# Kernel optimization log

Hardware: AMD Instinct MI355X
Metric: run time of the kernel (lower is better)

## Reference

```python
import jax, jax.numpy as jnp
import numpy as np

C = 256
R = 16  # reduction
CR = C // R
LN_EPS = 1e-5


def setup_inputs() -> dict:
    key = jax.random.key(0)
    ks = jax.random.split(key, 8)
    B, H, W = 16, 128, 128
    x = jax.random.normal(ks[0], (B, C, H, W), dtype=jnp.float32)
    # conv_mask: Conv2d(C, 1, 1x1)
    w_mask = jax.random.normal(ks[1], (C,), dtype=jnp.float32) * (1.0 / np.sqrt(C))
    b_mask = jnp.zeros((), dtype=jnp.float32)
    # channel_add[0]: Conv2d(C, C//R, 1x1)
    w1 = jax.random.normal(ks[2], (CR, C), dtype=jnp.float32) * (1.0 / np.sqrt(C))
    b1 = jnp.zeros((CR,), dtype=jnp.float32)
    # channel_add[1]: LayerNorm([C//R, 1, 1])
    ln_g = jnp.ones((CR,), dtype=jnp.float32)
    ln_b = jnp.zeros((CR,), dtype=jnp.float32)
    # channel_add[3]: Conv2d(C//R, C, 1x1)
    w2 = jax.random.normal(ks[3], (C, CR), dtype=jnp.float32) * (1.0 / np.sqrt(CR))
    b2 = jnp.zeros((C,), dtype=jnp.float32)
    return {"x": x, "w_mask": w_mask, "b_mask": b_mask,
            "w1": w1, "b1": b1, "ln_g": ln_g, "ln_b": ln_b,
            "w2": w2, "b2": b2}


def reference(x, w_mask, b_mask, w1, b1, ln_g, ln_b, w2, b2):
    B, Cc, H, W = x.shape
    # 1x1 conv to 1 channel -> attention logits over H*W
    logits = jnp.einsum('bchw,c->bhw', x, w_mask) + b_mask          # [B,H,W]
    attn = jax.nn.softmax(logits.reshape(B, H * W), axis=-1)        # [B,HW]
    # attention-pooled global context: [B,C]
    context = jnp.einsum('bchw,bs->bc', x, attn.reshape(B, H, W).reshape(B, H * W)[:, :].reshape(B, H * W)) if False else jnp.einsum('bcs,bs->bc', x.reshape(B, Cc, H * W), attn)
    # channel_add MLP: conv1x1 -> LayerNorm over [C//R] -> ReLU -> conv1x1
    t = jnp.einsum('oc,bc->bo', w1, context) + b1                   # [B,C//R]
    mu = jnp.mean(t, axis=-1, keepdims=True)
    var = jnp.mean((t - mu) ** 2, axis=-1, keepdims=True)
    t = (t - mu) / jnp.sqrt(var + LN_EPS) * ln_g + ln_b
    t = jax.nn.relu(t)
    add = jnp.einsum('oc,bc->bo', w2, t) + b2                       # [B,C]
    return x + add[:, :, None, None]
```

## Files before the change

kernel.cpp:

```cpp
#include <hip/hip_runtime.h>
#include <hip/hip_bf16.h>
#include <math.h>

#define CC   256
#define CR   16
#define SB   16384
#define NB   16
#define NCHUNK 64
#define CHSZ  256
#define ST   64
#define NT   (SB/ST)
#define LN_EPS 1e-5f

typedef float          vfloat4  __attribute__((ext_vector_type(4)));
typedef unsigned short vushort4 __attribute__((ext_vector_type(4)));

__device__ __forceinline__ unsigned short f2b(float f) {
    __hip_bfloat16 h = __float2bfloat16(f);
    unsigned short u;
    __builtin_memcpy(&u, &h, 2);
    return u;
}
__device__ __forceinline__ float b2f(unsigned short u) {
    unsigned int v = ((unsigned int)u) << 16;
    float f;
    __builtin_memcpy(&f, &v, 4);
    return f;
}

__global__ __launch_bounds__(256) void k1_shadow_part(const float* __restrict__ x,
                                                      const float* __restrict__ w_mask,
                                                      __hip_bfloat16* __restrict__ xb16,
                                                      float* __restrict__ part) {
    const int t   = threadIdx.x;
    const int bid = blockIdx.x;
    const int sq  = bid & 15;
    const int cg  = (bid >> 4) & 15;
    const int b   = bid >> 8;

    __shared__ float wm[16];
    if (t < 16) wm[t] = w_mask[cg * 16 + t];
    __syncthreads();

    const int s = sq * 1024 + t * 4;
    const size_t base = ((size_t)b * CC + (size_t)cg * 16) * SB + s;

    vfloat4 v[16];
#pragma unroll
    for (int c = 0; c < 16; ++c)
        v[c] = __builtin_nontemporal_load(
            reinterpret_cast<const vfloat4*>(x + base + (size_t)c * SB));

    float ax = 0.f, ay = 0.f, az = 0.f, aw = 0.f;
#pragma unroll
    for (int c = 0; c < 16; ++c) {
        const float w = wm[c];
        ax += w * v[c].x; ay += w * v[c].y; az += w * v[c].z; aw += w * v[c].w;
    }

#pragma unroll
    for (int c = 0; c < 16; ++c) {
        vushort4 u = { f2b(v[c].x), f2b(v[c].y), f2b(v[c].z), f2b(v[c].w) };
        *reinterpret_cast<vushort4*>(xb16 + base + (size_t)c * SB) = u;
    }
    vfloat4 acc = { ax, ay, az, aw };
    *reinterpret_cast<vfloat4*>(part + ((size_t)b * 16 + cg) * SB + s) = acc;
}

__global__ __launch_bounds__(256) void k2_chunks(const float* __restrict__ part,
                                                 float* __restrict__ pl_num,
                                                 float* __restrict__ pm,
                                                 float* __restrict__ ps) {
    const int t  = threadIdx.x;
    const int b  = blockIdx.x >> 6;
    const int ch = blockIdx.x & 63;
    __shared__ float red[256];

    const int s = ch * CHSZ + t;
    float l = 0.f;
#pragma unroll
    for (int cg = 0; cg < 16; ++cg)
        l += __builtin_nontemporal_load(part + ((size_t)b * 16 + cg) * SB + s);

    red[t] = l; __syncthreads();
    for (int st = 128; st > 0; st >>= 1) {
        if (t < st) red[t] = fmaxf(red[t], red[t + st]);
        __syncthreads();
    }
    const float mc = red[0]; __syncthreads();

    const float p = __expf(l - mc);
    pl_num[(size_t)b * SB + s] = p;

    red[t] = p; __syncthreads();
    for (int st = 128; st > 0; st >>= 1) {
        if (t < st) red[t] += red[t + st];
        __syncthreads();
    }
    if (t == 0) { pm[b * NCHUNK + ch] = mc; ps[b * NCHUNK + ch] = red[0]; }
}

__global__ __launch_bounds__(256) void k3_context(const __hip_bfloat16* __restrict__ xb16,
                                                  const float* __restrict__ pl_num,
                                                  const float* __restrict__ pm,
                                                  const float* __restrict__ ps,
                                                  float* __restrict__ ctx) {
    const int t = threadIdx.x;
    const int b = blockIdx.x >> 8;
    const int c = blockIdx.x & 255;
    __shared__ float fxs[NCHUNK];
    __shared__ float red[256];

    if (t < NCHUNK) {
        const float m_t = pm[b * NCHUNK + t];
        float M = m_t;
#pragma unroll
        for (int off = 32; off > 0; off >>= 1)
            M = fmaxf(M, __shfl_xor(M, off));
        const float f = __expf(m_t - M);
        float z = ps[b * NCHUNK + t] * f;
#pragma unroll
        for (int off = 32; off > 0; off >>= 1)
            z += __shfl_xor(z, off);
        fxs[t] = f / z;
    }
    __syncthreads();

    const __hip_bfloat16* row = xb16 + ((size_t)b * CC + c) * SB;
    const float* pn = pl_num + (size_t)b * SB;

    float acc = 0.f;
#pragma unroll
    for (int k = 0; k < 16; ++k) {
        const int s = k * 1024 + t * 4;
        const ushort4 u = *reinterpret_cast<const ushort4*>(row + s);
        const float4 p = *reinterpret_cast<const float4*>(pn + s);
        const float f = fxs[(k << 2) + (t >> 6)];
        acc += f * (b2f(u.x) * p.x + b2f(u.y) * p.y + b2f(u.z) * p.z + b2f(u.w) * p.w);
    }
    red[t] = acc; __syncthreads();
    for (int st = 128; st > 0; st >>= 1) {
        if (t < st) red[t] += red[t + st];
        __syncthreads();
    }
    if (t == 0) ctx[(size_t)b * CC + c] = red[0];
}

__global__ __launch_bounds__(256) void k4_mlp(const float* __restrict__ ctx,
                                              const float* __restrict__ w1,
                                              const float* __restrict__ b1,
                                              const float* __restrict__ ln_g,
                                              const float* __restrict__ ln_b,
                                              const float* __restrict__ w2,
                                              const float* __restrict__ b2,
                                              float* __restrict__ add) {
    const int b = blockIdx.x;
    const int t = threadIdx.x;
    __shared__ float cx[CC];
    __shared__ float tbuf[CR];
    __shared__ float tn[CR];

    cx[t] = ctx[(size_t)b * CC + t];
    __syncthreads();

    if (t < CR) {
        float a = b1[t];
        const float* w1r = w1 + (size_t)t * CC;
#pragma unroll 8
        for (int c = 0; c < CC; ++c) a += w1r[c] * cx[c];
        tbuf[t] = a;
    }
    __syncthreads();
    if (t == 0) {
        float mu = 0.f;
        for (int q = 0; q < CR; ++q) mu += tbuf[q];
        mu *= (1.0f / CR);
        float var = 0.f;
        for (int q = 0; q < CR; ++q) { const float d = tbuf[q] - mu; var += d * d; }
        var *= (1.0f / CR);
        const float inv = rsqrtf(var + LN_EPS);
        for (int q = 0; q < CR; ++q) {
            const float v = (tbuf[q] - mu) * inv * ln_g[q] + ln_b[q];
            tn[q] = v > 0.f ? v : 0.f;
        }
    }
    __syncthreads();

    float a = b2[t];
    const float* w2r = w2 + (size_t)t * CR;
#pragma unroll
    for (int o = 0; o < CR; ++o) a += w2r[o] * tn[o];
    add[(size_t)b * CC + t] = a;
}

__global__ __launch_bounds__(256) void k5_add(const __hip_bfloat16* __restrict__ xb16,
                                              const float* __restrict__ add,
                                              float* __restrict__ out) {
    const size_t idx = ((size_t)blockIdx.x * 256 + threadIdx.x) * 8;
    const size_t bc = idx / SB;
    const float a = add[bc];
    const uint4 d = *reinterpret_cast<const uint4*>(xb16 + idx);
    vfloat4 o0 = {b2f(d.x & 0xffffu) + a, b2f(d.x >> 16) + a,
                  b2f(d.y & 0xffffu) + a, b2f(d.y >> 16) + a};
    vfloat4 o1 = {b2f(d.z & 0xffffu) + a, b2f(d.z >> 16) + a,
                  b2f(d.w & 0xffffu) + a, b2f(d.w >> 16) + a};
    __builtin_nontemporal_store(o0, reinterpret_cast<vfloat4*>(out + idx));
    __builtin_nontemporal_store(o1, reinterpret_cast<vfloat4*>(out + idx + 4));
}

__global__ __launch_bounds__(256) void f_ctx_partial(const float* __restrict__ x,
                                                     const float* __restrict__ w_mask,
                                                     float* __restrict__ pc,
                                                     float* __restrict__ pm,
                                                     float* __restrict__ ps) {
    __shared__ float plog[ST * 5];
    __shared__ float pl[ST];
    __shared__ float wm[CC];
    __shared__ float red2[CC * 17];

    const int t   = threadIdx.x;
    const int bid = blockIdx.x;
    const int b   = bid / NT;
    const int s0  = (bid % NT) * ST;

    wm[t] = w_mask[t];
    __syncthreads();

    const int g  = t >> 4;
    const int i  = t & 15;
    const int s4 = i << 2;

    const float* xb = x + (size_t)b * CC * SB + s0 + s4;
    float4 v[16];
    float4 acc = make_float4(0.f, 0.f, 0.f, 0.f);
#pragma unroll
    for (int k = 0; k < 16; ++k) {
        const int c = g + (k << 4);
        v[k] = *reinterpret_cast<const float4*>(xb + (size_t)c * SB);
        const float w = wm[c];
        acc.x += v[k].x * w; acc.y += v[k].y * w;
        acc.z += v[k].z * w; acc.w += v[k].w * w;
    }
    acc.x += __shfl_xor(acc.x, 16); acc.y += __shfl_xor(acc.y, 16);
    acc.z += __shfl_xor(acc.z, 16); acc.w += __shfl_xor(acc.w, 16);
    acc.x += __shfl_xor(acc.x, 32); acc.y += __shfl_xor(acc.y, 32);
    acc.z += __shfl_xor(acc.z, 32); acc.w += __shfl_xor(acc.w, 32);
    const int wv = t >> 6;
    if ((t & 63) < 16) {
        plog[(s4 + 0) * 5 + wv] = acc.x;
        plog[(s4 + 1) * 5 + wv] = acc.y;
        plog[(s4 + 2) * 5 + wv] = acc.z;
        plog[(s4 + 3) * 5 + wv] = acc.w;
    }
    __syncthreads();

    if (t < ST) {
        const float logit = plog[t * 5 + 0] + plog[t * 5 + 1]
                          + plog[t * 5 + 2] + plog[t * 5 + 3];
        float m = logit;
#pragma unroll
        for (int off = 32; off > 0; off >>= 1)
            m = fmaxf(m, __shfl_xor(m, off));
        const float p = __expf(logit - m);
        pl[t] = p;
        float sum = p;
#pragma unroll
        for (int off = 32; off > 0; off >>= 1)
            sum += __shfl_xor(sum, off);
        if (t == 0) { pm[bid] = m; ps[bid] = sum; }
    }
    __syncthreads();

    const float p0 = pl[s4 + 0], p1 = pl[s4 + 1];
    const float p2 = pl[s4 + 2], p3 = pl[s4 + 3];
#pragma unroll
    for (int k = 0; k < 16; ++k) {
        const int c = g + (k << 4);
        red2[c * 17 + i] = v[k].x * p0 + v[k].y * p1 + v[k].z * p2 + v[k].w * p3;
    }
    __syncthreads();
    float s = 0.f;
#pragma unroll
    for (int j = 0; j < 16; ++j) s += red2[t * 17 + j];
    pc[(size_t)bid * CC + t] = s;
}

__global__ __launch_bounds__(256) void f_combine_mlp(const float* __restrict__ pc,
                                                     const float* __restrict__ pm,
                                                     const float* __restrict__ ps,
                                                     const float* __restrict__ w1,
                                                     const float* __restrict__ b1,
                                                     const float* __restrict__ ln_g,
                                                     const float* __restrict__ ln_b,
                                                     const float* __restrict__ w2,
                                                     const float* __restrict__ b2,
                                                     float* __restrict__ add) {
    const int b = blockIdx.x;
    const int t = threadIdx.x;
    __shared__ float red[256];
    __shared__ float fx[NT];
    __shared__ float ctx[CC];
    __shared__ float tbuf[CR];
    __shared__ float tn[CR];

    const float m_t = pm[b * NT + t];
    red[t] = m_t; __syncthreads();
    for (int st = 128; st > 0; st >>= 1) {
        if (t < st) red[t] = fmaxf(red[t], red[t + st]);
        __syncthreads();
    }
    const float M = red[0]; __syncthreads();

    const float f = __expf(m_t - M);
    fx[t] = f;
    red[t] = ps[b * NT + t] * f; __syncthreads();
    for (int st = 128; st > 0; st >>= 1) {
        if (t < st) red[t] += red[t + st];
        __syncthreads();
    }
    const float invZ = 1.0f / red[0]; __syncthreads();

    float acc = 0.f;
#pragma unroll 4
    for (int j = 0; j < NT; ++j)
        acc += pc[((size_t)b * NT + j) * CC + t] * fx[j];
    ctx[t] = acc * invZ;
    __syncthreads();

    if (t < CR) {
        float a = b1[t];
        const float* w1r = w1 + (size_t)t * CC;
#pragma unroll 8
        for (int c = 0; c < CC; ++c) a += w1r[c] * ctx[c];
        tbuf[t] = a;
    }
    __syncthreads();
    if (t == 0) {
        float mu = 0.f;
        for (int i = 0; i < CR; ++i) mu += tbuf[i];
        mu *= (1.0f / CR);
        float var = 0.f;
        for (int i = 0; i < CR; ++i) { const float d = tbuf[i] - mu; var += d * d; }
        var *= (1.0f / CR);
        const float inv = rsqrtf(var + LN_EPS);
        for (int i = 0; i < CR; ++i) {
            const float v = (tbuf[i] - mu) * inv * ln_g[i] + ln_b[i];
            tn[i] = v > 0.f ? v : 0.f;
        }
    }
    __syncthreads();

    float a = b2[t];
    const float* w2r = w2 + (size_t)t * CR;
#pragma unroll
    for (int o = 0; o < CR; ++o) a += w2r[o] * tn[o];
    add[(size_t)b * CC + t] = a;
}

__global__ __launch_bounds__(256) void f_add(const float* __restrict__ x,
                                             const float* __restrict__ add,
                                             float* __restrict__ out) {
    const size_t idx = ((size_t)blockIdx.x * 256 + threadIdx.x) * 8;
    const size_t bc = idx / SB;
    const float a = add[bc];
    const float4 v0 = *reinterpret_cast<const float4*>(x + idx);
    const float4 v1 = *reinterpret_cast<const float4*>(x + idx + 4);
    vfloat4 o0 = {v0.x + a, v0.y + a, v0.z + a, v0.w + a};
    vfloat4 o1 = {v1.x + a, v1.y + a, v1.z + a, v1.w + a};
    __builtin_nontemporal_store(o0, reinterpret_cast<vfloat4*>(out + idx));
    __builtin_nontemporal_store(o1, reinterpret_cast<vfloat4*>(out + idx + 4));
}

extern "C" void kernel_launch(void* const* d_in, const int* in_sizes, int n_in,
                              void* d_out, int out_size, void* d_ws, size_t ws_size,
                              hipStream_t stream) {
    const float* x      = (const float*)d_in[0];
    const float* w_mask = (const float*)d_in[1];
    const float* w1     = (const float*)d_in[3];
    const float* b1     = (const float*)d_in[4];
    const float* ln_g   = (const float*)d_in[5];
    const float* ln_b   = (const float*)d_in[6];
    const float* w2     = (const float*)d_in[7];
    const float* b2     = (const float*)d_in[8];
    float* out = (float*)d_out;

    const size_t nx = (size_t)NB * CC * SB;
    __hip_bfloat16* xb16 = (__hip_bfloat16*)d_ws;
    float* fbase  = (float*)((char*)d_ws + nx * sizeof(__hip_bfloat16));
    float* part   = fbase;
    float* pl_num = part + (size_t)NB * 16 * SB;
    float* pm     = pl_num + (size_t)NB * SB;
    float* ps     = pm + NB * NCHUNK;
    float* ctx    = ps + NB * NCHUNK;
    float* add    = ctx + (size_t)NB * CC;
    const size_t need = (size_t)((char*)(add + (size_t)NB * CC) - (char*)d_ws);

    if (ws_size >= need) {
        k1_shadow_part<<<dim3(NB * 256), dim3(256), 0, stream>>>(x, w_mask, xb16, part);
        k2_chunks<<<dim3(NB * NCHUNK), dim3(256), 0, stream>>>(part, pl_num, pm, ps);
        k3_context<<<dim3(NB * CC), dim3(256), 0, stream>>>(xb16, pl_num, pm, ps, ctx);
        k4_mlp<<<dim3(NB), dim3(256), 0, stream>>>(ctx, w1, b1, ln_g, ln_b, w2, b2, add);
        k5_add<<<dim3(32768), dim3(256), 0, stream>>>(xb16, add, out);
    } else {
        float* pc  = (float*)d_ws;
        float* fpm = pc + (size_t)NB * NT * CC;
        float* fps = fpm + (size_t)NB * NT;
        float* fad = fps + (size_t)NB * NT;
        f_ctx_partial<<<dim3(NB * NT), dim3(256), 0, stream>>>(x, w_mask, pc, fpm, fps);
        f_combine_mlp<<<dim3(NB), dim3(256), 0, stream>>>(pc, fpm, fps, w1, b1, ln_g, ln_b, w2, b2, fad);
        f_add<<<dim3(NB * CC * SB / 2048), dim3(256), 0, stream>>>(x, fad, out);
    }
}
```

Baseline: 199.5 us.

## Store bf16 shadow in per-block tile layout and tile context and add kernels

The bf16 shadow copy of x is now written in a block-contiguous tile layout: each 16-channel by 1024-position tile is one contiguous 32 KB chunk. The context and add kernels are re-tiled to use the same 4096-block decomposition. The context kernel now emits 16 per-channel partial sums per tile using wave shuffles instead of a full LDS tree reduction, and the MLP kernel sums those partials. Other changes: a hand-written round-to-nearest-even bf16 conversion, and plain loads in place of nontemporal loads on x and the partial logits. The aim is more contiguous streaming and fewer reduction barriers. The cost is an extra partial-sum buffer, and the cache behaviour may change now that the nontemporal hints are gone.

Result: faster. 175.3 us (-12.2%).

```diff
diff --git a/kernel.cpp b/kernel.cpp
--- a/kernel.cpp
+++ b/kernel.cpp
@@ -1,5 +1,4 @@
 #include <hip/hip_runtime.h>
-#include <hip/hip_bf16.h>
 #include <math.h>
 
 #define CC   256
@@ -16,10 +15,11 @@
 typedef unsigned short vushort4 __attribute__((ext_vector_type(4)));
 
 __device__ __forceinline__ unsigned short f2b(float f) {
-    __hip_bfloat16 h = __float2bfloat16(f);
-    unsigned short u;
-    __builtin_memcpy(&u, &h, 2);
-    return u;
+    unsigned int u;
+    __builtin_memcpy(&u, &f, 4);
+    unsigned int lsb = (u >> 16) & 1u;
+    u += 0x7fffu + lsb;
+    return (unsigned short)(u >> 16);
 }
 __device__ __forceinline__ float b2f(unsigned short u) {
     unsigned int v = ((unsigned int)u) << 16;
@@ -30,7 +30,7 @@
 
 __global__ __launch_bounds__(256) void k1_shadow_part(const float* __restrict__ x,
                                                       const float* __restrict__ w_mask,
-                                                      __hip_bfloat16* __restrict__ xb16,
+                                                      unsigned short* __restrict__ shadow,
                                                       float* __restrict__ part) {
     const int t   = threadIdx.x;
     const int bid = blockIdx.x;
@@ -42,14 +42,12 @@
     if (t < 16) wm[t] = w_mask[cg * 16 + t];
     __syncthreads();
 
-    const int s = sq * 1024 + t * 4;
-    const size_t base = ((size_t)b * CC + (size_t)cg * 16) * SB + s;
+    const size_t xbase = ((size_t)b * CC + cg * 16) * SB + sq * 1024 + t * 4;
 
     vfloat4 v[16];
 #pragma unroll
     for (int c = 0; c < 16; ++c)
-        v[c] = __builtin_nontemporal_load(
-            reinterpret_cast<const vfloat4*>(x + base + (size_t)c * SB));
+        v[c] = *reinterpret_cast<const vfloat4*>(x + xbase + (size_t)c * SB);
 
     float ax = 0.f, ay = 0.f, az = 0.f, aw = 0.f;
 #pragma unroll
@@ -58,13 +56,14 @@
         ax += w * v[c].x; ay += w * v[c].y; az += w * v[c].z; aw += w * v[c].w;
     }
 
+    unsigned short* chunk = shadow + (size_t)bid * 16384 + t * 4;
 #pragma unroll
     for (int c = 0; c < 16; ++c) {
         vushort4 u = { f2b(v[c].x), f2b(v[c].y), f2b(v[c].z), f2b(v[c].w) };
-        *reinterpret_cast<vushort4*>(xb16 + base + (size_t)c * SB) = u;
+        *reinterpret_cast<vushort4*>(chunk + c * 1024) = u;
     }
     vfloat4 acc = { ax, ay, az, aw };
-    *reinterpret_cast<vfloat4*>(part + ((size_t)b * 16 + cg) * SB + s) = acc;
+    *reinterpret_cast<vfloat4*>(part + ((size_t)b * 16 + cg) * SB + sq * 1024 + t * 4) = acc;
 }
 
 __global__ __launch_bounds__(256) void k2_chunks(const float* __restrict__ part,
@@ -80,7 +79,7 @@
     float l = 0.f;
 #pragma unroll
     for (int cg = 0; cg < 16; ++cg)
-        l += __builtin_nontemporal_load(part + ((size_t)b * 16 + cg) * SB + s);
+        l += part[((size_t)b * 16 + cg) * SB + s];
 
     red[t] = l; __syncthreads();
     for (int st = 128; st > 0; st >>= 1) {
@@ -100,16 +99,19 @@
     if (t == 0) { pm[b * NCHUNK + ch] = mc; ps[b * NCHUNK + ch] = red[0]; }
 }
 
-__global__ __launch_bounds__(256) void k3_context(const __hip_bfloat16* __restrict__ xb16,
+__global__ __launch_bounds__(256) void k3_context(const unsigned short* __restrict__ shadow,
                                                   const float* __restrict__ pl_num,
                                                   const float* __restrict__ pm,
                                                   const float* __restrict__ ps,
-                                                  float* __restrict__ ctx) {
-    const int t = threadIdx.x;
-    const int b = blockIdx.x >> 8;
-    const int c = blockIdx.x & 255;
-    __shared__ float fxs[NCHUNK];
-    __shared__ float red[256];
+                                                  float* __restrict__ ctxp) {
+    const int t   = threadIdx.x;
+    const int bid = blockIdx.x;
+    const int sq  = bid & 15;
+    const int cg  = (bid >> 4) & 15;
+    const int b   = bid >> 8;
+
+    __shared__ float fxs[4];
+    __shared__ float wred[4][16];
 
     if (t < NCHUNK) {
         const float m_t = pm[b * NCHUNK + t];
@@ -122,31 +124,39 @@
 #pragma unroll
         for (int off = 32; off > 0; off >>= 1)
             z += __shfl_xor(z, off);
-        fxs[t] = f / z;
-    }
-    __syncthreads();
-
-    const __hip_bfloat16* row = xb16 + ((size_t)b * CC + c) * SB;
-    const float* pn = pl_num + (size_t)b * SB;
-
-    float acc = 0.f;
-#pragma unroll
-    for (int k = 0; k < 16; ++k) {
-        const int s = k * 1024 + t * 4;
-        const ushort4 u = *reinterpret_cast<const ushort4*>(row + s);
-        const float4 p = *reinterpret_cast<const float4*>(pn + s);
-        const float f = fxs[(k << 2) + (t >> 6)];
-        acc += f * (b2f(u.x) * p.x + b2f(u.y) * p.y + b2f(u.z) * p.z + b2f(u.w) * p.w);
-    }
-    red[t] = acc; __syncthreads();
-    for (int st = 128; st > 0; st >>= 1) {
-        if (t < st) red[t] += red[t + st];
-        __syncthreads();
-    }
-    if (t == 0) ctx[(size_t)b * CC + c] = red[0];
-}
-
-__global__ __launch_bounds__(256) void k4_mlp(const float* __restrict__ ctx,
+        const int rel = t - sq * 4;
+        if (rel >= 0 && rel < 4) fxs[rel] = f / z;
+    }
+    __syncthreads();
+
+    const unsigned short* chunk = shadow + (size_t)bid * 16384;
+    float4 p = *reinterpret_cast<const float4*>(pl_num + (size_t)b * SB + sq * 1024 + t * 4);
+    const float f = fxs[t >> 6];
+    p.x *= f; p.y *= f; p.z *= f; p.w *= f;
+
+    float acc[16];
+#pragma unroll
+    for (int c = 0; c < 16; ++c) {
+        const ushort4 u = *reinterpret_cast<const ushort4*>(chunk + c * 1024 + t * 4);
+        acc[c] = b2f(u.x) * p.x + b2f(u.y) * p.y + b2f(u.z) * p.z + b2f(u.w) * p.w;
+    }
+#pragma unroll
+    for (int c = 0; c < 16; ++c) {
+#pragma unroll
+        for (int off = 32; off > 0; off >>= 1)
+            acc[c] += __shfl_xor(acc[c], off);
+    }
+    const int wv = t >> 6;
+    if ((t & 63) == 0) {
+#pragma unroll
+        for (int c = 0; c < 16; ++c) wred[wv][c] = acc[c];
+    }
+    __syncthreads();
+    if (t < 16)
+        ctxp[(size_t)bid * 16 + t] = wred[0][t] + wred[1][t] + wred[2][t] + wred[3][t];
+}
+
+__global__ __launch_bounds__(256) void k4_mlp(const float* __restrict__ ctxp,
                                               const float* __restrict__ w1,
                                               const float* __restrict__ b1,
                                               const float* __restrict__ ln_g,
@@ -160,7 +170,14 @@
     __shared__ float tbuf[CR];
     __shared__ float tn[CR];
 
-    cx[t] = ctx[(size_t)b * CC + t];
+    {
+        const int cg = t >> 4, c = t & 15;
+        float s = 0.f;
+#pragma unroll
+        for (int sq = 0; sq < 16; ++sq)
+            s += ctxp[(((size_t)b * 16 + cg) * 16 + sq) * 16 + c];
+        cx[t] = s;
+    }
     __syncthreads();
 
     if (t < CR) {
@@ -193,19 +210,32 @@
     add[(size_t)b * CC + t] = a;
 }
 
-__global__ __launch_bounds__(256) void k5_add(const __hip_bfloat16* __restrict__ xb16,
+__global__ __launch_bounds__(256) void k5_add(const unsigned short* __restrict__ shadow,
                                               const float* __restrict__ add,
                                               float* __restrict__ out) {
-    const size_t idx = ((size_t)blockIdx.x * 256 + threadIdx.x) * 8;
-    const size_t bc = idx / SB;
-    const float a = add[bc];
-    const uint4 d = *reinterpret_cast<const uint4*>(xb16 + idx);
-    vfloat4 o0 = {b2f(d.x & 0xffffu) + a, b2f(d.x >> 16) + a,
-                  b2f(d.y & 0xffffu) + a, b2f(d.y >> 16) + a};
-    vfloat4 o1 = {b2f(d.z & 0xffffu) + a, b2f(d.z >> 16) + a,
-                  b2f(d.w & 0xffffu) + a, b2f(d.w >> 16) + a};
-    __builtin_nontemporal_store(o0, reinterpret_cast<vfloat4*>(out + idx));
-    __builtin_nontemporal_store(o1, reinterpret_cast<vfloat4*>(out + idx + 4));
+    const int t   = threadIdx.x;
+    const int bid = blockIdx.x;
+    const int sq  = bid & 15;
+    const int cg  = (bid >> 4) & 15;
+    const int b   = bid >> 8;
+
+    __shared__ float adds[16];
+    if (t < 16) adds[t] = add[(size_t)b * CC + cg * 16 + t];
+    __syncthreads();
+
+    const unsigned short* chunk = shadow + (size_t)bid * 16384 + t * 4;
+    ushort4 u[16];
+#pragma unroll
+    for (int c = 0; c < 16; ++c)
+        u[c] = *reinterpret_cast<const ushort4*>(chunk + c * 1024);
+
+    float* ob = out + ((size_t)b * CC + cg * 16) * SB + sq * 1024 + t * 4;
+#pragma unroll
+    for (int c = 0; c < 16; ++c) {
+        const float a = adds[c];
+        vfloat4 o = { b2f(u[c].x) + a, b2f(u[c].y) + a, b2f(u[c].z) + a, b2f(u[c].w) + a };
+        __builtin_nontemporal_store(o, reinterpret_cast<vfloat4*>(ob + (size_t)c * SB));
+    }
 }
 
 __global__ __launch_bounds__(256) void f_ctx_partial(const float* __restrict__ x,
@@ -385,22 +415,22 @@
     float* out = (float*)d_out;
 
     const size_t nx = (size_t)NB * CC * SB;
-    __hip_bfloat16* xb16 = (__hip_bfloat16*)d_ws;
-    float* fbase  = (float*)((char*)d_ws + nx * sizeof(__hip_bfloat16));
+    unsigned short* shadow = (unsigned short*)d_ws;
+    float* fbase  = (float*)((char*)d_ws + nx * sizeof(unsigned short));
     float* part   = fbase;
     float* pl_num = part + (size_t)NB * 16 * SB;
     float* pm     = pl_num + (size_t)NB * SB;
     float* ps     = pm + NB * NCHUNK;
-    float* ctx    = ps + NB * NCHUNK;
-    float* add    = ctx + (size_t)NB * CC;
+    float* ctxp   = ps + NB * NCHUNK;
+    float* add    = ctxp + (size_t)NB * 16 * 16 * 16;
     const size_t need = (size_t)((char*)(add + (size_t)NB * CC) - (char*)d_ws);
 
     if (ws_size >= need) {
-        k1_shadow_part<<<dim3(NB * 256), dim3(256), 0, stream>>>(x, w_mask, xb16, part);
+        k1_shadow_part<<<dim3(4096), dim3(256), 0, stream>>>(x, w_mask, shadow, part);
         k2_chunks<<<dim3(NB * NCHUNK), dim3(256), 0, stream>>>(part, pl_num, pm, ps);
-        k3_context<<<dim3(NB * CC), dim3(256), 0, stream>>>(xb16, pl_num, pm, ps, ctx);
-        k4_mlp<<<dim3(NB), dim3(256), 0, stream>>>(ctx, w1, b1, ln_g, ln_b, w2, b2, add);
-        k5_add<<<dim3(32768), dim3(256), 0, stream>>>(xb16, add, out);
+        k3_context<<<dim3(4096), dim3(256), 0, stream>>>(shadow, pl_num, pm, ps, ctxp);
+        k4_mlp<<<dim3(NB), dim3(256), 0, stream>>>(ctxp, w1, b1, ln_g, ln_b, w2, b2, add);
+        k5_add<<<dim3(4096), dim3(256), 0, stream>>>(shadow, add, out);
     } else {
         float* pc  = (float*)d_ws;
         float* fpm = pc + (size_t)NB * NT * CC;
```
